# Kernel optimization log

Measured on AMD Instinct MI355X. Metric: run time of the kernel, lower is better.

## Reference

```python
import jax, jax.numpy as jnp
import numpy as np

B, G, P = 4096, 31, 8
C = P * (P + 1) // 2  # 36 pairwise-with-replacement combinations


def setup_inputs() -> dict:
    key = jax.random.key(0)
    k1, k2 = jax.random.split(key)
    param_tensor = jax.random.normal(k1, (B, G, G, P), dtype=jnp.float32)
    integral_coeffs = jax.random.normal(k2, (G, G, C), dtype=jnp.float32)
    return {"param_tensor": param_tensor, "integral_coeffs": integral_coeffs}


def reference(param_tensor, integral_coeffs):
    # torch.combinations(param, 2, with_replacement=True).prod(-1) over last dim
    # == param[ii] * param[jj] for upper-triangular-with-diagonal index pairs.
    P_ = param_tensor.shape[-1]
    ii, jj = np.triu_indices(P_)  # same ordering as torch.combinations with_replacement
    pairs = param_tensor[..., ii] * param_tensor[..., jj]  # [B, G, G, C]
    # weight by per-cell coeffs, sum over pair dim and over both grid dims -> [B]
    return jnp.einsum('bghc,ghc->b', pairs, integral_coeffs)
```

## Files before the change

kernel.cpp:

```cpp
#include <hip/hip_runtime.h>

#define B_  4096
#define G_  31
#define GG_ 961
#define P_  8
#define C_  36
#define R_  16

__global__ void zero_kernel(float* out, int n) {
    int i = blockIdx.x * blockDim.x + threadIdx.x;
    if (i < n) out[i] = 0.0f;
}

__global__ __launch_bounds__(256, 4)
void quadform_kernel(const float* __restrict__ param,
                     const float* __restrict__ coef,
                     float* __restrict__ out) {
    const int lane    = threadIdx.x & 63;
    const int wv      = threadIdx.x >> 6;
    const int gh_tile = blockIdx.x * 4 + wv;
    const int gh      = gh_tile * 64 + lane;
    const bool valid  = gh < GG_;
    const int  ghc    = valid ? gh : (GG_ - 1);

    float cf[C_];
    const float4* cp = reinterpret_cast<const float4*>(coef) + (size_t)ghc * (C_ / 4);
    #pragma unroll
    for (int q = 0; q < C_ / 4; ++q) {
        float4 v = cp[q];
        cf[4*q+0] = v.x; cf[4*q+1] = v.y; cf[4*q+2] = v.z; cf[4*q+3] = v.w;
    }
    if (!valid) {
        #pragma unroll
        for (int c = 0; c < C_; ++c) cf[c] = 0.0f;
    }

    const int b0 = blockIdx.y * R_;
    const float4* pb = reinterpret_cast<const float4*>(param);
    size_t idx = ((size_t)b0 * GG_ + ghc) * 2;
    float4 p0 = pb[idx];
    float4 p1 = pb[idx + 1];

    for (int r = 0; r < R_; ++r) {
        const float pv[P_] = {p0.x, p0.y, p0.z, p0.w, p1.x, p1.y, p1.z, p1.w};
        if (r + 1 < R_) {
            size_t nx = idx + (size_t)(r + 1) * (GG_ * 2);
            p0 = pb[nx];
            p1 = pb[nx + 1];
        }
        float s = 0.0f;
        int c = 0;
        #pragma unroll
        for (int i = 0; i < P_; ++i) {
            #pragma unroll
            for (int j = i; j < P_; ++j) {
                s = fmaf(cf[c] * pv[i], pv[j], s);
                ++c;
            }
        }
        #pragma unroll
        for (int off = 32; off; off >>= 1) s += __shfl_xor(s, off, 64);
        if (lane == 0) atomicAdd(&out[b0 + r], s);
    }
}

extern "C" void kernel_launch(void* const* d_in, const int* in_sizes, int n_in,
                              void* d_out, int out_size, void* d_ws, size_t ws_size,
                              hipStream_t stream) {
    const float* param = (const float*)d_in[0];
    const float* coef  = (const float*)d_in[1];
    float* out = (float*)d_out;

    zero_kernel<<<(B_ + 255) / 256, 256, 0, stream>>>(out, B_);

    dim3 grid(4, B_ / R_);
    quadform_kernel<<<grid, 256, 0, stream>>>(param, coef, out);
}
```

Before: 186.0 us.

## Issue all batch-row loads upfront and batch wave reductions across rows

Halves the batch rows per block from 16 to 8 and loads all 8 rows of parameters into registers before computing, replacing the one-row-ahead prefetch loop. This exposes more memory-level parallelism per thread so load latency is not serialized. The 8 per-row sums are then reduced together with interleaved shuffles and written with 8 atomics. In exchange, register pressure rises and the grid doubles, so each block's coefficient loads are reused over fewer rows.

```diff
diff --git a/kernel.cpp b/kernel.cpp
--- a/kernel.cpp
+++ b/kernel.cpp
@@ -5,7 +5,7 @@
 #define GG_ 961
 #define P_  8
 #define C_  36
-#define R_  16
+#define R_  8
 
 __global__ void zero_kernel(float* out, int n) {
     int i = blockIdx.x * blockDim.x + threadIdx.x;
@@ -24,11 +24,13 @@
     const int  ghc    = valid ? gh : (GG_ - 1);
 
     float cf[C_];
-    const float4* cp = reinterpret_cast<const float4*>(coef) + (size_t)ghc * (C_ / 4);
-    #pragma unroll
-    for (int q = 0; q < C_ / 4; ++q) {
-        float4 v = cp[q];
-        cf[4*q+0] = v.x; cf[4*q+1] = v.y; cf[4*q+2] = v.z; cf[4*q+3] = v.w;
+    {
+        const float4* cp = reinterpret_cast<const float4*>(coef) + (size_t)ghc * (C_ / 4);
+        #pragma unroll
+        for (int q = 0; q < C_ / 4; ++q) {
+            float4 v = cp[q];
+            cf[4*q+0] = v.x; cf[4*q+1] = v.y; cf[4*q+2] = v.z; cf[4*q+3] = v.w;
+        }
     }
     if (!valid) {
         #pragma unroll
@@ -37,30 +39,52 @@
 
     const int b0 = blockIdx.y * R_;
     const float4* pb = reinterpret_cast<const float4*>(param);
-    size_t idx = ((size_t)b0 * GG_ + ghc) * 2;
-    float4 p0 = pb[idx];
-    float4 p1 = pb[idx + 1];
+    const size_t base = ((size_t)b0 * GG_ + ghc) * 2;
+    const size_t bstep = (size_t)GG_ * 2;
 
-    for (int r = 0; r < R_; ++r) {
-        const float pv[P_] = {p0.x, p0.y, p0.z, p0.w, p1.x, p1.y, p1.z, p1.w};
-        if (r + 1 < R_) {
-            size_t nx = idx + (size_t)(r + 1) * (GG_ * 2);
-            p0 = pb[nx];
-            p1 = pb[nx + 1];
+    float4 qa[4][2], qb[4][2];
+    #pragma unroll
+    for (int r = 0; r < 4; ++r) {
+        qa[r][0] = pb[base + (size_t)r * bstep];
+        qa[r][1] = pb[base + (size_t)r * bstep + 1];
+    }
+    #pragma unroll
+    for (int r = 0; r < 4; ++r) {
+        qb[r][0] = pb[base + (size_t)(r + 4) * bstep];
+        qb[r][1] = pb[base + (size_t)(r + 4) * bstep + 1];
+    }
+
+    float s[R_];
+    #pragma unroll
+    for (int h = 0; h < 2; ++h) {
+        #pragma unroll
+        for (int r = 0; r < 4; ++r) {
+            float4 p0 = h ? qb[r][0] : qa[r][0];
+            float4 p1 = h ? qb[r][1] : qa[r][1];
+            const float pv[P_] = {p0.x, p0.y, p0.z, p0.w, p1.x, p1.y, p1.z, p1.w};
+            float acc = 0.0f;
+            int c = 0;
+            #pragma unroll
+            for (int i = 0; i < P_; ++i) {
+                #pragma unroll
+                for (int j = i; j < P_; ++j) {
+                    acc = fmaf(cf[c] * pv[i], pv[j], acc);
+                    ++c;
+                }
+            }
+            s[h * 4 + r] = acc;
         }
-        float s = 0.0f;
-        int c = 0;
+    }
+
+    #pragma unroll
+    for (int off = 32; off; off >>= 1) {
         #pragma unroll
-        for (int i = 0; i < P_; ++i) {
-            #pragma unroll
-            for (int j = i; j < P_; ++j) {
-                s = fmaf(cf[c] * pv[i], pv[j], s);
-                ++c;
-            }
-        }
+        for (int r = 0; r < R_; ++r) s[r] += __shfl_xor(s[r], off, 64);
+    }
+
+    if (lane == 0) {
         #pragma unroll
-        for (int off = 32; off; off >>= 1) s += __shfl_xor(s, off, 64);
-        if (lane == 0) atomicAdd(&out[b0 + r], s);
+        for (int r = 0; r < R_; ++r) atomicAdd(&out[b0 + r], s[r]);
     }
 }
 
```

Result: no change. 184.0 us (-1.1%).
